# Performance work log

Hardware: AMD Instinct MI355X
Metric: run time of the kernel (lower is better)

The kernel has to match this reference:

```python
import jax, jax.numpy as jnp
import numpy as np

NEG_INF = -jnp.inf


def conv2d(x, w, b, stride, pad):
    # x: [B,C,H,W], w: [O,I,kh,kw]
    y = jax.lax.conv_general_dilated(
        x, w, window_strides=(stride, stride),
        padding=[(pad, pad), (pad, pad)],
        dimension_numbers=('NCHW', 'OIHW', 'NCHW'))
    return y + b[None, :, None, None]


def maxpool3s2(x):
    return jax.lax.reduce_window(x, -jnp.inf, jax.lax.max,
                                 (1, 1, 3, 3), (1, 1, 2, 2), 'VALID')


def setup_inputs() -> dict:
    key = jax.random.key(0)
    ks = jax.random.split(key, 20)
    s = 0.02
    B, C, H, W = 64, 3, 224, 224
    D, HID, OUT, E = 9216, 288, 1000, 8   # feature_dim, hidden_dim, output_dim, n_experts
    GH = 72                               # gate hidden = hidden_dim // 4
    inp = {
        'x':   jax.random.normal(ks[0], (B, C, H, W), jnp.float32),
        'c1w': s * jax.random.normal(ks[1], (64, 3, 11, 11), jnp.float32),
        'c1b': jnp.zeros((64,), jnp.float32),
        'c2w': s * jax.random.normal(ks[2], (192, 64, 5, 5), jnp.float32),
        'c2b': jnp.zeros((192,), jnp.float32),
        'c3w': s * jax.random.normal(ks[3], (384, 192, 3, 3), jnp.float32),
        'c3b': jnp.zeros((384,), jnp.float32),
        'c4w': s * jax.random.normal(ks[4], (256, 384, 3, 3), jnp.float32),
        'c4b': jnp.zeros((256,), jnp.float32),
        'c5w': s * jax.random.normal(ks[5], (256, 256, 3, 3), jnp.float32),
        'c5b': jnp.zeros((256,), jnp.float32),
        'gw1': s * jax.random.normal(ks[6], (D, GH), jnp.float32),
        'gb1': jnp.zeros((GH,), jnp.float32),
        'gw2': s * jax.random.normal(ks[7], (GH, E), jnp.float32),
        'gb2': jnp.zeros((E,), jnp.float32),
        'ew1': s * jax.random.normal(ks[8], (E, D, HID), jnp.float32),
        'eb1': jnp.zeros((E, HID), jnp.float32),
        'ew2': s * jax.random.normal(ks[9], (E, HID, HID // 2), jnp.float32),
        'eb2': jnp.zeros((E, HID // 2), jnp.float32),
        'ew3': s * jax.random.normal(ks[10], (E, HID // 2, OUT), jnp.float32),
        'eb3': jnp.zeros((E, OUT), jnp.float32),
    }
    return inp


def reference(x, c1w, c1b, c2w, c2b, c3w, c3b, c4w, c4b, c5w, c5b,
              gw1, gb1, gw2, gb2, ew1, eb1, ew2, eb2, ew3, eb3):
    # ---- AlexNet-style feature extractor (224 branch) ----
    h = jax.nn.relu(conv2d(x, c1w, c1b, 4, 2))   # [B,64,55,55]
    h = maxpool3s2(h)                             # [B,64,27,27]
    h = jax.nn.relu(conv2d(h, c2w, c2b, 1, 2))   # [B,192,27,27]
    h = maxpool3s2(h)                             # [B,192,13,13]
    h = jax.nn.relu(conv2d(h, c3w, c3b, 1, 1))   # [B,384,13,13]
    h = jax.nn.relu(conv2d(h, c4w, c4b, 1, 1))   # [B,256,13,13]
    h = jax.nn.relu(conv2d(h, c5w, c5b, 1, 1))   # [B,256,13,13]
    h = maxpool3s2(h)                             # [B,256,6,6]
    # AdaptiveAvgPool2d((6,6)) on a 6x6 input is the identity.
    feat = h.reshape(h.shape[0], -1)              # [B,9216]

    # ---- Gate: top-2 routing (eval mode: no noise, no dropout) ----
    g = jax.nn.relu(feat @ gw1 + gb1)             # [B,72]
    logits = g @ gw2 + gb2                        # [B,8]
    topv, topi = jax.lax.top_k(logits, 2)         # [B,2]
    topw = jax.nn.softmax(topv, axis=-1)          # softmax over top-2 only
    B = logits.shape[0]
    gates = jnp.zeros_like(logits).at[jnp.arange(B)[:, None], topi].set(topw)  # [B,8]

    # ---- Dense per-expert 3-layer MLP over full batch (as in source) ----
    h1 = jax.nn.relu(jnp.einsum('bd,edh->ebh', feat, ew1) + eb1[:, None, :])   # [E,B,288]
    h2 = jax.nn.relu(jnp.einsum('ebh,ehk->ebk', h1, ew2) + eb2[:, None, :])    # [E,B,144]
    eo = jnp.einsum('ebk,eko->ebo', h2, ew3) + eb3[:, None, :]                 # [E,B,1000]
    # Weighted combine; gates are zero for non-top-2 experts, matching the
    # masked accumulation loop in the torch forward.
    out = jnp.einsum('ebo,be->bo', eo, gates)     # [B,1000]
    return out
```

## Files before the change

kernel.cpp:

```cpp
#include <hip/hip_runtime.h>
#include <math.h>

#define TPB 256

typedef short s16x8 __attribute__((ext_vector_type(8)));
typedef short s16x4 __attribute__((ext_vector_type(4)));
typedef float f32x4 __attribute__((ext_vector_type(4)));

__device__ inline void bsplit(float x, short& h, short& l){
  union { float f; unsigned u; } a, hf, rf;
  a.f = x;
  unsigned hu = (a.u + 0x7FFFu + ((a.u >> 16) & 1u)) >> 16;
  h = (short)hu;
  hf.u = hu << 16;
  rf.f = x - hf.f;
  l = (short)((rf.u + 0x7FFFu + ((rf.u >> 16) & 1u)) >> 16);
}
__device__ inline float b2f(short s){
  union { unsigned u; float f; } x;
  x.u = ((unsigned)(unsigned short)s) << 16;
  return x.f;
}

__global__ __launch_bounds__(TPB) void wsplit_k(
    const float* __restrict__ w, short* __restrict__ wh, short* __restrict__ wl,
    int C, int O, int ntap, int total)
{
  int idx = blockIdx.x*TPB + threadIdx.x;
  if (idx >= total) return;
  int c   = idx % C;
  int t2  = idx / C;
  int oc  = t2 % O;
  int tap = t2 / O;
  float x = w[((size_t)oc*C + c)*ntap + tap];
  short h, l; bsplit(x, h, l);
  int tile = oc >> 4, ln = oc & 15;
  int S    = ntap*(C >> 5);
  int sl   = tap*(C >> 5) + (c >> 5);
  int lg   = (c >> 3) & 3, j = c & 7;
  size_t dst = (((size_t)tile*S + sl)*64 + lg*16 + ln)*8 + j;
  wh[dst] = h; wl[dst] = l;
}

__global__ __launch_bounds__(TPB) void wsplit1_k(
    const float* __restrict__ w, short* __restrict__ wh, short* __restrict__ wl)
{
  int idx = blockIdx.x*TPB + threadIdx.x;
  if (idx >= 64*576) return;
  int k  = idx % 576;
  int oc = idx / 576;
  int g  = k >> 4, kw = k & 15;
  int c  = g / 12, kh = g % 12;
  float x = 0.f;
  if (kh < 11 && kw < 11)
    x = w[((size_t)oc*3 + c)*121 + kh*11 + kw];
  short h, l; bsplit(x, h, l);
  int m = oc >> 4, ln = oc & 15;
  int s = k >> 5, r = k & 31;
  int lg = r >> 3, j = r & 7;
  size_t dst = (((size_t)m*18 + s)*64 + lg*16 + ln)*8 + j;
  wh[dst] = h; wl[dst] = l;
}

__global__ __launch_bounds__(TPB) void wtrans_k(
    const float* __restrict__ w, float* __restrict__ wT, int K, int O)
{
  int idx = blockIdx.x*TPB + threadIdx.x;
  if (idx >= K*O) return;
  int oc = idx % O;
  int k  = idx / O;
  wT[idx] = w[(size_t)oc*K + k];
}

#define C1W 240
__global__ __launch_bounds__(256, 2) void conv1p_k(
    const float* __restrict__ in, const short* __restrict__ whi,
    const short* __restrict__ wlo, const float* __restrict__ bias,
    short* __restrict__ yh, short* __restrict__ yl)
{
  __shared__ __align__(16) short lds[2][57*C1W + 84];
  const int tid = threadIdx.x;
  const int r  = blockIdx.x;
  const int b  = blockIdx.y;
  const int nt = tid >> 6;
  const int ln = tid & 15;
  const int lg = (tid & 63) >> 4;
  const int lane = tid & 63;
  const int ow = nt*16 + ln;

  const float* ip = in + (size_t)b*3*224*224;
  for (int i = tid; i < 57*59; i += 256){
    int plane = i / 59;
    int p     = i % 59;
    int c = plane / 19, ri = plane % 19;
    int ih = 8*r - 2 + ri;
    int col0 = p*4;
    const float* rowp = (ih >= 0 && ih < 224) ? ip + (size_t)c*50176 + (size_t)ih*224 : nullptr;
    short h[4], l[4];
    #pragma unroll
    for (int j=0;j<4;++j){
      int iw = col0 + j - 2;
      float v = (rowp && iw >= 0 && iw < 224) ? rowp[iw] : 0.f;
      bsplit(v, h[j], l[j]);
    }
    s16x4 hv = {h[0],h[1],h[2],h[3]}, lv = {l[0],l[1],l[2],l[3]};
    *reinterpret_cast<s16x4*>(&lds[0][plane*C1W + col0]) = hv;
    *reinterpret_cast<s16x4*>(&lds[1][plane*C1W + col0]) = lv;
  }
  __syncthreads();

  f32x4 acc[3][4];
  #pragma unroll
  for (int m=0;m<4;++m){
    const float4 bv = *reinterpret_cast<const float4*>(bias + m*16 + lg*4);
    #pragma unroll
    for (int sub=0;sub<3;++sub)
      acc[sub][m] = (f32x4){bv.x, bv.y, bv.z, bv.w};
  }

  s16x8 ah[4], al[4], ahn[4], aln[4];
  #pragma unroll
  for (int m=0;m<4;++m){
    size_t ao = (((size_t)m*18 + 0)*64 + lane)*8;
    ah[m] = *reinterpret_cast<const s16x8*>(whi + ao);
    al[m] = *reinterpret_cast<const s16x8*>(wlo + ao);
  }

  #pragma unroll 1
  for (int s=0; s<18; ++s){
    if (s < 17){
      #pragma unroll
      for (int m=0;m<4;++m){
        size_t ao = (((size_t)m*18 + s + 1)*64 + lane)*8;
        ahn[m] = *reinterpret_cast<const s16x8*>(whi + ao);
        aln[m] = *reinterpret_cast<const s16x8*>(wlo + ao);
      }
    }
    int g  = 2*s + (lg >> 1);
    int c  = g / 12, kh = g % 12;
    int khp = (kh < 11) ? kh : 10;
    #pragma unroll
    for (int sub=0;sub<3;++sub){
      int plane = c*19 + 4*sub + khp;
      int base  = plane*C1W + ow*4 + (lg & 1)*8;
      s16x4 h0 = *reinterpret_cast<const s16x4*>(&lds[0][base]);
      s16x4 h1 = *reinterpret_cast<const s16x4*>(&lds[0][base+4]);
      s16x4 l0 = *reinterpret_cast<const s16x4*>(&lds[1][base]);
      s16x4 l1 = *reinterpret_cast<const s16x4*>(&lds[1][base+4]);
      s16x8 bh = __builtin_shufflevector(h0, h1, 0,1,2,3,4,5,6,7);
      s16x8 bl = __builtin_shufflevector(l0, l1, 0,1,2,3,4,5,6,7);
      #pragma unroll
      for (int m=0;m<4;++m){
        acc[sub][m] = __builtin_amdgcn_mfma_f32_16x16x32_bf16(al[m], bh, acc[sub][m], 0,0,0);
        acc[sub][m] = __builtin_amdgcn_mfma_f32_16x16x32_bf16(ah[m], bl, acc[sub][m], 0,0,0);
        acc[sub][m] = __builtin_amdgcn_mfma_f32_16x16x32_bf16(ah[m], bh, acc[sub][m], 0,0,0);
      }
    }
    #pragma unroll
    for (int m=0;m<4;++m){ ah[m] = ahn[m]; al[m] = aln[m]; }
  }

  __syncthreads();
  float* convbuf = (float*)&lds[0][0];
  if (ow < 55){
    #pragma unroll
    for (int sub=0;sub<3;++sub)
      #pragma unroll
      for (int m=0;m<4;++m)
        #pragma unroll
        for (int rr=0;rr<4;++rr){
          int oc = m*16 + lg*4 + rr;
          convbuf[(sub*64 + oc)*57 + ow] = fmaxf(acc[sub][m][rr], 0.f);
        }
  }
  __syncthreads();

  for (int i = tid; i < 27*64; i += 256){
    int pw = i >> 6, c = i & 63;
    float m = -INFINITY;
    #pragma unroll
    for (int sub=0;sub<3;++sub)
      #pragma unroll
      for (int j=0;j<3;++j)
        m = fmaxf(m, convbuf[(sub*64 + c)*57 + 2*pw + j]);
    short h, l; bsplit(m, h, l);
    size_t o = ((size_t)b*729 + r*27 + pw)*64 + c;
    yh[o] = h; yl[o] = l;
  }
}

__global__ __launch_bounds__(256, 3) void conv2m_k(
    const short* __restrict__ xh, const short* __restrict__ xl,
    const short* __restrict__ whi, const short* __restrict__ wlo,
    const float* __restrict__ bias, short* __restrict__ yh, short* __restrict__ yl)
{
  __shared__ __align__(16) short lds[2][217*40];
  const int tid = threadIdx.x;
  const int rg  = blockIdx.x;
  const int b   = blockIdx.y;
  const int wid = tid >> 6;
  const int ln  = tid & 15;
  const int lg  = (tid & 63) >> 4;
  const int lane = tid & 63;
  const int oc0 = wid*48;
  const int r0  = rg*3;

  int sb[6], nn[6];
  #pragma unroll
  for (int t=0;t<6;++t){
    int n = t*16 + ln;
    nn[t] = n;
    int ohl = n / 27, ow = n % 27;
    sb[t] = (n < 81) ? (ohl*31 + ow) : 0;
  }

  f32x4 acc[3][6];
  #pragma unroll
  for (int m=0;m<3;++m){
    const float4 bv = *reinterpret_cast<const float4*>(bias + oc0 + m*16 + lg*4);
    #pragma unroll
    for (int t=0;t<6;++t) acc[m][t] = (f32x4){bv.x, bv.y, bv.z, bv.w};
  }

  #pragma unroll 1
  for (int c0=0; c0<64; c0+=32){
    __syncthreads();
    for (int i = tid; i < 217*4; i += 256){
      int sp = i >> 2, v = i & 3;
      int pr = sp/31, pc = sp%31;
      int ih = r0 - 2 + pr, iw = pc - 2;
      s16x8 hv = {0,0,0,0,0,0,0,0}, lv = {0,0,0,0,0,0,0,0};
      if (ih >= 0 && ih < 27 && iw >= 0 && iw < 27){
        size_t o = ((size_t)b*729 + ih*27 + iw)*64 + c0 + v*8;
        hv = *reinterpret_cast<const s16x8*>(xh + o);
        lv = *reinterpret_cast<const s16x8*>(xl + o);
      }
      *reinterpret_cast<s16x8*>(&lds[0][sp*40 + v*8]) = hv;
      *reinterpret_cast<s16x8*>(&lds[1][sp*40 + v*8]) = lv;
    }
    __syncthreads();

    const size_t tstr = 50*512;
    const size_t abase = ((size_t)(wid*3)*50 + (c0 >> 5))*512 + (size_t)lane*8;
    s16x8 ah0 = *reinterpret_cast<const s16x8*>(whi + abase);
    s16x8 ah1 = *reinterpret_cast<const s16x8*>(whi + abase + tstr);
    s16x8 ah2 = *reinterpret_cast<const s16x8*>(whi + abase + 2*tstr);
    s16x8 al0 = *reinterpret_cast<const s16x8*>(wlo + abase);
    s16x8 al1 = *reinterpret_cast<const s16x8*>(wlo + abase + tstr);
    s16x8 al2 = *reinterpret_cast<const s16x8*>(wlo + abase + 2*tstr);

    #pragma unroll 1
    for (int tap=0; tap<25; ++tap){
      s16x8 nh0=ah0, nh1=ah1, nh2=ah2, nl0=al0, nl1=al1, nl2=al2;
      if (tap < 24){
        size_t ao = abase + (size_t)(tap+1)*2*512;
        nh0 = *reinterpret_cast<const s16x8*>(whi + ao);
        nh1 = *reinterpret_cast<const s16x8*>(whi + ao + tstr);
        nh2 = *reinterpret_cast<const s16x8*>(whi + ao + 2*tstr);
        nl0 = *reinterpret_cast<const s16x8*>(wlo + ao);
        nl1 = *reinterpret_cast<const s16x8*>(wlo + ao + tstr);
        nl2 = *reinterpret_cast<const s16x8*>(wlo + ao + 2*tstr);
      }
      const int toff = (tap/5)*31 + (tap%5);
      #pragma unroll
      for (int t=0;t<6;++t){
        int off = (sb[t] + toff)*40 + lg*8;
        s16x8 bh = *reinterpret_cast<const s16x8*>(&lds[0][off]);
        s16x8 bl = *reinterpret_cast<const s16x8*>(&lds[1][off]);
        acc[0][t] = __builtin_amdgcn_mfma_f32_16x16x32_bf16(al0, bh, acc[0][t], 0,0,0);
        acc[0][t] = __builtin_amdgcn_mfma_f32_16x16x32_bf16(ah0, bl, acc[0][t], 0,0,0);
        acc[0][t] = __builtin_amdgcn_mfma_f32_16x16x32_bf16(ah0, bh, acc[0][t], 0,0,0);
        acc[1][t] = __builtin_amdgcn_mfma_f32_16x16x32_bf16(al1, bh, acc[1][t], 0,0,0);
        acc[1][t] = __builtin_amdgcn_mfma_f32_16x16x32_bf16(ah1, bl, acc[1][t], 0,0,0);
        acc[1][t] = __builtin_amdgcn_mfma_f32_16x16x32_bf16(ah1, bh, acc[1][t], 0,0,0);
        acc[2][t] = __builtin_amdgcn_mfma_f32_16x16x32_bf16(al2, bh, acc[2][t], 0,0,0);
        acc[2][t] = __builtin_amdgcn_mfma_f32_16x16x32_bf16(ah2, bl, acc[2][t], 0,0,0);
        acc[2][t] = __builtin_amdgcn_mfma_f32_16x16x32_bf16(ah2, bh, acc[2][t], 0,0,0);
      }
      ah0=nh0; ah1=nh1; ah2=nh2; al0=nl0; al1=nl1; al2=nl2;
    }
  }

  #pragma unroll
  for (int m=0;m<3;++m)
    #pragma unroll
    for (int t=0;t<6;++t){
      if (nn[t] < 81){
        int gsp = r0*27 + nn[t];
        size_t base = ((size_t)b*729 + gsp)*192 + oc0 + m*16 + lg*4;
        short h[4], l[4];
        #pragma unroll
        for (int r=0;r<4;++r) bsplit(fmaxf(acc[m][t][r], 0.f), h[r], l[r]);
        s16x4 hv = {h[0],h[1],h[2],h[3]}, lv = {l[0],l[1],l[2],l[3]};
        *reinterpret_cast<s16x4*>(yh + base) = hv;
        *reinterpret_cast<s16x4*>(yl + base) = lv;
      }
    }
}

__global__ __launch_bounds__(TPB) void pool2_k(
    const short* __restrict__ xh, const short* __restrict__ xl,
    short* __restrict__ yh, short* __restrict__ yl)
{
  int i = blockIdx.x*TPB + threadIdx.x;
  if (i >= 64*169*192) return;
  int c = i % 192;
  int t = i / 192;
  int sp = t % 169;
  int b = t / 169;
  int r = sp/13, cc = sp%13;
  const short* ph = xh + (size_t)b*729*192 + c;
  const short* pl = xl + (size_t)b*729*192 + c;
  float m = -INFINITY;
  #pragma unroll
  for (int di=0;di<3;++di)
    #pragma unroll
    for (int dj=0;dj<3;++dj){
      size_t s = (size_t)((2*r+di)*27 + 2*cc+dj)*192;
      m = fmaxf(m, b2f(ph[s]) + b2f(pl[s]));
    }
  short h, l; bsplit(m, h, l);
  yh[i] = h; yl[i] = l;
}

template<int C,int O>
__global__ __launch_bounds__(256, 3) void conv3m_k(
    const short* __restrict__ xh, const short* __restrict__ xl,
    const short* __restrict__ whi, const short* __restrict__ wlo,
    const float* __restrict__ bias, short* __restrict__ yh, short* __restrict__ yl)
{
  __shared__ __align__(16) short lds[2][225*40];
  const int tid = threadIdx.x;
  const int b   = blockIdx.y;
  const int wid = tid >> 6;
  const int ln  = tid & 15;
  const int lg  = (tid & 63) >> 4;
  const int lane = tid & 63;
  const int tileIdx = blockIdx.x*2 + (wid & 1);
  const int oc0 = tileIdx*16;
  const int ng  = wid >> 1;
  const int tbase  = ng ? 6 : 0;
  const int ntiles = ng ? 5 : 6;
  const int S3 = 9*(C/32);

  int sb[6], nn[6];
  #pragma unroll
  for (int t=0;t<6;++t){
    int n = (tbase + t)*16 + ln;
    nn[t] = n;
    int oh = n / 13, ow = n % 13;
    sb[t] = (n < 169) ? (oh*15 + ow) : 0;
  }

  f32x4 acc[6];
  const float4 bv = *reinterpret_cast<const float4*>(bias + oc0 + lg*4);
  #pragma unroll
  for (int t=0;t<6;++t) acc[t] = (f32x4){bv.x, bv.y, bv.z, bv.w};

  #pragma unroll 1
  for (int c0=0; c0<C; c0+=32){
    __syncthreads();
    for (int i = tid; i < 225*4; i += 256){
      int sp = i >> 2, v = i & 3;
      int r = sp/15, cc = sp%15;
      s16x8 hv = {0,0,0,0,0,0,0,0}, lv = {0,0,0,0,0,0,0,0};
      if (r >= 1 && r <= 13 && cc >= 1 && cc <= 13){
        size_t o = ((size_t)b*169 + (r-1)*13 + (cc-1))*C + c0 + v*8;
        hv = *reinterpret_cast<const s16x8*>(xh + o);
        lv = *reinterpret_cast<const s16x8*>(xl + o);
      }
      *reinterpret_cast<s16x8*>(&lds[0][sp*40 + v*8]) = hv;
      *reinterpret_cast<s16x8*>(&lds[1][sp*40 + v*8]) = lv;
    }
    __syncthreads();

    const size_t tb = (size_t)tileIdx*S3 + (c0 >> 5);
    s16x8 ah = *reinterpret_cast<const s16x8*>(whi + (tb*64 + lane)*8);
    s16x8 al = *reinterpret_cast<const s16x8*>(wlo + (tb*64 + lane)*8);
    #pragma unroll 1
    for (int tap=0; tap<9; ++tap){
      s16x8 ahn = ah, aln = al;
      if (tap < 8){
        size_t ao = ((tb + (size_t)(tap+1)*(C/32))*64 + lane)*8;
        ahn = *reinterpret_cast<const s16x8*>(whi + ao);
        aln = *reinterpret_cast<const s16x8*>(wlo + ao);
      }
      const int toff = (tap/3)*15 + (tap%3);
      #pragma unroll
      for (int t=0;t<6;++t){
        if (t < ntiles){
          int off = (sb[t] + toff)*40 + lg*8;
          s16x8 bh = *reinterpret_cast<const s16x8*>(&lds[0][off]);
          s16x8 bl = *reinterpret_cast<const s16x8*>(&lds[1][off]);
          acc[t] = __builtin_amdgcn_mfma_f32_16x16x32_bf16(al, bh, acc[t], 0,0,0);
          acc[t] = __builtin_amdgcn_mfma_f32_16x16x32_bf16(ah, bl, acc[t], 0,0,0);
          acc[t] = __builtin_amdgcn_mfma_f32_16x16x32_bf16(ah, bh, acc[t], 0,0,0);
        }
      }
      ah = ahn; al = aln;
    }
  }

  #pragma unroll
  for (int t=0;t<6;++t){
    if (t < ntiles && nn[t] < 169){
      size_t base = ((size_t)b*169 + nn[t])*O + oc0 + lg*4;
      short h[4], l[4];
      #pragma unroll
      for (int r=0;r<4;++r) bsplit(fmaxf(acc[t][r], 0.f), h[r], l[r]);
      s16x4 hv = {h[0],h[1],h[2],h[3]}, lv = {l[0],l[1],l[2],l[3]};
      *reinterpret_cast<s16x4*>(yh + base) = hv;
      *reinterpret_cast<s16x4*>(yl + base) = lv;
    }
  }
}

__global__ __launch_bounds__(TPB) void pool3_k(
    const short* __restrict__ xh, const short* __restrict__ xl,
    float* __restrict__ feat)
{
  int i = blockIdx.x*TPB + threadIdx.x;
  if (i >= 64*9216) return;
  int d = i % 9216;
  int b = i / 9216;
  int c = d / 36;
  int sp = d % 36;
  int r = sp/6, cc = sp%6;
  const short* ph = xh + (size_t)b*169*256 + c;
  const short* pl = xl + (size_t)b*169*256 + c;
  float m = -INFINITY;
  #pragma unroll
  for (int di=0;di<3;++di)
    #pragma unroll
    for (int dj=0;dj<3;++dj){
      size_t s = (size_t)((2*r+di)*13 + 2*cc+dj)*256;
      m = fmaxf(m, b2f(ph[s]) + b2f(pl[s]));
    }
  feat[i] = m;
}

__global__ __launch_bounds__(TPB) void featsplit_k(
    const float* __restrict__ feat, short* __restrict__ fbh, short* __restrict__ fbl)
{
  int idx = blockIdx.x*TPB + threadIdx.x;
  if (idx >= 589824) return;
  int j = idx & 7;
  int lane = (idx >> 3) & 63;
  int nt = (idx >> 9) & 3;
  int s = idx >> 11;
  int b = nt*16 + (lane & 15);
  int d = s*32 + (lane >> 4)*8 + j;
  short h, l; bsplit(feat[(size_t)b*9216 + d], h, l);
  fbh[idx] = h; fbl[idx] = l;
}

__global__ __launch_bounds__(256) void gate1_k(
    const float* __restrict__ feat, const float* __restrict__ gw1T,
    const float* __restrict__ gb1, float* __restrict__ g)
{
  const int b    = blockIdx.x;
  const int h    = blockIdx.y*4 + (threadIdx.x >> 6);
  const int lane = threadIdx.x & 63;
  const float* f = feat + (size_t)b*9216;
  const float* w = gw1T + (size_t)h*9216;
  float s = 0.f;
  #pragma unroll
  for (int it=0; it<36; ++it){
    int d = it*256 + lane*4;
    float4 fv = *reinterpret_cast<const float4*>(f + d);
    float4 wv = *reinterpret_cast<const float4*>(w + d);
    s = fmaf(fv.x, wv.x, s);
    s = fmaf(fv.y, wv.y, s);
    s = fmaf(fv.z, wv.z, s);
    s = fmaf(fv.w, wv.w, s);
  }
  #pragma unroll
  for (int off=32; off; off>>=1) s += __shfl_down(s, off, 64);
  if (lane == 0) g[(size_t)b*72 + h] = fmaxf(s + gb1[h], 0.f);
}

__global__ __launch_bounds__(128) void gate2_k(
    const float* __restrict__ g, const float* __restrict__ gw2,
    const float* __restrict__ gb2, float* __restrict__ gates)
{
  const int b = blockIdx.x;
  const int tid = threadIdx.x;
  __shared__ float gs[72];
  __shared__ float logits[8];
  if (tid < 72) gs[tid] = g[(size_t)b*72 + tid];
  __syncthreads();
  if (tid < 8) {
    float acc = gb2[tid];
    for (int j=0;j<72;++j)
      acc = fmaf(gs[j], gw2[(size_t)j*8 + tid], acc);
    logits[tid] = acc;
  }
  __syncthreads();
  if (tid == 0) {
    int i1 = 0; float v1 = logits[0];
    for (int e=1;e<8;++e) if (logits[e] > v1) { v1 = logits[e]; i1 = e; }
    int i2 = -1; float v2 = -INFINITY;
    for (int e=0;e<8;++e) { if (e==i1) continue; if (logits[e] > v2) { v2 = logits[e]; i2 = e; } }
    float z  = expf(v2 - v1);
    float w1 = 1.f / (1.f + z);
    float w2 = z   / (1.f + z);
    float* gr = gates + (size_t)b*8;
    for (int e=0;e<8;++e) gr[e] = 0.f;
    gr[i1] = w1;
    gr[i2] = w2;
  }
}

__global__ __launch_bounds__(256, 4) void eh1m_k(
    const float* __restrict__ ew1, const short* __restrict__ fbh,
    const short* __restrict__ fbl, float* __restrict__ part)
{
  __shared__ __align__(16) short wh_l[32*88];
  __shared__ __align__(16) short wl_l[32*88];
  const int m2 = blockIdx.x;
  const int e  = blockIdx.y;
  const int ks = blockIdx.z;
  const int tid = threadIdx.x;
  const int nt = tid >> 6;
  const int ln = tid & 15;
  const int lg = (tid & 63) >> 4;
  const int lane = tid & 63;

  f32x4 acc[2] = {(f32x4){0.f,0.f,0.f,0.f},(f32x4){0.f,0.f,0.f,0.f}};

  const float* wsrc = ew1 + (size_t)e*9216*288 + (size_t)m2*32;
  const int d0 = ks*576;

  #pragma unroll 1
  for (int st=0; st<9; ++st){
    __syncthreads();
    {
      int drow = tid >> 2;
      int h0 = (tid & 3)*8;
      const float* src = wsrc + (size_t)(d0 + st*64 + drow)*288 + h0;
      float4 v0 = *reinterpret_cast<const float4*>(src);
      float4 v1 = *reinterpret_cast<const float4*>(src+4);
      float vv[8] = {v0.x,v0.y,v0.z,v0.w,v1.x,v1.y,v1.z,v1.w};
      #pragma unroll
      for (int k=0;k<8;++k){
        short h, l; bsplit(vv[k], h, l);
        wh_l[(h0+k)*88 + drow] = h;
        wl_l[(h0+k)*88 + drow] = l;
      }
    }
    __syncthreads();
    int sg = (d0 + st*64) >> 5;
    #pragma unroll
    for (int sl=0; sl<2; ++sl){
      size_t bo = ((size_t)(sg+sl)*4 + nt)*512 + (size_t)lane*8;
      s16x8 bh = *reinterpret_cast<const s16x8*>(fbh + bo);
      s16x8 bl = *reinterpret_cast<const s16x8*>(fbl + bo);
      #pragma unroll
      for (int m=0;m<2;++m){
        int ao = (m*16 + ln)*88 + sl*32 + lg*8;
        s16x8 ah = *reinterpret_cast<const s16x8*>(&wh_l[ao]);
        s16x8 al = *reinterpret_cast<const s16x8*>(&wl_l[ao]);
        acc[m] = __builtin_amdgcn_mfma_f32_16x16x32_bf16(al, bh, acc[m], 0,0,0);
        acc[m] = __builtin_amdgcn_mfma_f32_16x16x32_bf16(ah, bl, acc[m], 0,0,0);
        acc[m] = __builtin_amdgcn_mfma_f32_16x16x32_bf16(ah, bh, acc[m], 0,0,0);
      }
    }
  }
  #pragma unroll
  for (int m=0;m<2;++m){
    int h = m2*32 + m*16 + lg*4;
    int b = nt*16 + ln;
    float* pp = part + ((size_t)(ks*8+e)*288 + h)*64 + b;
    #pragma unroll
    for (int r=0;r<4;++r)
      pp[(size_t)r*64] = acc[m][r];
  }
}

__global__ __launch_bounds__(TPB) void eh1_reduce_k(
    const float* __restrict__ part, const float* __restrict__ eb1,
    float* __restrict__ h1)
{
  int idx = blockIdx.x*TPB + threadIdx.x;
  if (idx >= 8*288*64) return;
  int b = idx & 63;
  int h = (idx >> 6) % 288;
  int e = idx / (64*288);
  float a = eb1[(size_t)e*288 + h];
  #pragma unroll
  for (int s=0;s<16;++s)
    a += part[((size_t)(s*8+e)*288 + h)*64 + b];
  h1[((size_t)e*64 + b)*288 + h] = fmaxf(a, 0.f);
}

__global__ __launch_bounds__(TPB) void expert_h2_k(
    const float* __restrict__ h1, const float* __restrict__ ew2,
    const float* __restrict__ eb2, const float* __restrict__ gates,
    float* __restrict__ h2)
{
  int idx = blockIdx.x*TPB + threadIdx.x;
  if (idx >= 8*64*144) return;
  int k = idx % 144;
  int t = idx / 144;
  int b = t % 64;
  int e = t / 64;
  if (gates[(size_t)b*8 + e] == 0.f) return;
  float acc = eb2[(size_t)e*144 + k];
  const float* h = h1 + ((size_t)e*64 + b)*288;
  const float* w = ew2 + (size_t)e*288*144 + k;
  for (int d=0; d<288; ++d)
    acc = fmaf(h[d], w[(size_t)d*144], acc);
  h2[idx] = fmaxf(acc, 0.f);
}

__global__ __launch_bounds__(TPB) void expert_out_k(
    const float* __restrict__ h2, const float* __restrict__ ew3,
    const float* __restrict__ eb3, const float* __restrict__ gates,
    float* __restrict__ out)
{
  int idx = blockIdx.x*TPB + threadIdx.x;
  if (idx >= 64*1000) return;
  int o = idx % 1000;
  int b = idx / 1000;
  float acc = 0.f;
  const float* gr = gates + (size_t)b*8;
  for (int e=0;e<8;++e){
    float ge = gr[e];
    if (ge == 0.f) continue;
    float a = eb3[(size_t)e*1000 + o];
    const float* h = h2 + ((size_t)e*64 + b)*144;
    const float* w = ew3 + (size_t)e*144*1000 + o;
    for (int k=0;k<144;++k)
      a = fmaf(h[k], w[(size_t)k*1000], a);
    acc = fmaf(ge, a, acc);
  }
  out[idx] = acc;
}

static inline int nblk(long long n){ return (int)((n + TPB - 1) / TPB); }

extern "C" void kernel_launch(void* const* d_in, const int* in_sizes, int n_in,
                              void* d_out, int out_size, void* d_ws, size_t ws_size,
                              hipStream_t stream)
{
  const float* x   = (const float*)d_in[0];
  const float* c1w = (const float*)d_in[1];  const float* c1b = (const float*)d_in[2];
  const float* c2w = (const float*)d_in[3];  const float* c2b = (const float*)d_in[4];
  const float* c3w = (const float*)d_in[5];  const float* c3b = (const float*)d_in[6];
  const float* c4w = (const float*)d_in[7];  const float* c4b = (const float*)d_in[8];
  const float* c5w = (const float*)d_in[9];  const float* c5b = (const float*)d_in[10];
  const float* gw1 = (const float*)d_in[11]; const float* gb1 = (const float*)d_in[12];
  const float* gw2 = (const float*)d_in[13]; const float* gb2 = (const float*)d_in[14];
  const float* ew1 = (const float*)d_in[15]; const float* eb1 = (const float*)d_in[16];
  const float* ew2 = (const float*)d_in[17]; const float* eb2 = (const float*)d_in[18];
  const float* ew3 = (const float*)d_in[19]; const float* eb3 = (const float*)d_in[20];
  float* out = (float*)d_out;

  float* W = (float*)d_ws;
  short* X3H = (short*)W;
  short* X3L = X3H + 8957952;
  short* X5H = (short*)W;
  short* X5L = X5H + 4153344;
  short* X7H = (short*)W;
  short* X7L = X7H + 2768896;
  float* feat  = W + 5000000;
  short* FBH   = (short*)(W + 5600000);
  short* FBL   = (short*)(W + 5900000);
  float* part  = W + 6300000;
  short* WH2 = (short*)(W +  9000000);
  short* WL2 = WH2 + 307200;
  short* WH3 = (short*)(W +  9320000);
  short* WL3 = WH3 + 663552;
  short* WH4 = (short*)(W + 10000000);
  short* WL4 = WH4 + 884736;
  short* WH5 = (short*)(W + 10900000);
  short* WL5 = WH5 + 589824;
  float* GT1 = W + 11500000;
  short* X2H = (short*)(W + 12390400);
  short* X2L = X2H + 2985984;
  short* X4H = (short*)(W + 12390400);
  short* X4L = X4H + 2076672;
  short* X6H = (short*)(W + 12390400);
  short* X6L = X6H + 2768896;
  float* gates = W + 14000000;
  float* h1    = gates + 512;
  float* h2    = h1 + 147456;
  float* gbuf  = h2 + 73728;
  short* WH1 = (short*)(W + 15400000);
  short* WL1 = WH1 + 36864;
  (void)ws_size; (void)in_sizes; (void)n_in; (void)out_size;

  wsplit1_k<<<nblk(64LL*576), TPB, 0, stream>>>(c1w, WH1, WL1);
  conv1p_k<<<dim3(27,64), 256, 0, stream>>>(x, WH1, WL1, c1b, X2H, X2L);
  wsplit_k<<<nblk(25LL*192*64),  TPB, 0, stream>>>(c2w, WH2, WL2,  64, 192, 25, 25*192*64);
  wsplit_k<<<nblk(9LL*384*192),  TPB, 0, stream>>>(c3w, WH3, WL3, 192, 384,  9, 9*384*192);
  wsplit_k<<<nblk(9LL*256*384),  TPB, 0, stream>>>(c4w, WH4, WL4, 384, 256,  9, 9*256*384);
  wsplit_k<<<nblk(9LL*256*256),  TPB, 0, stream>>>(c5w, WH5, WL5, 256, 256,  9, 9*256*256);
  wtrans_k<<<nblk(72LL*9216),    TPB, 0, stream>>>(gw1, GT1, 72, 9216);

  conv2m_k<<<dim3(9,64), 256, 0, stream>>>(X2H, X2L, WH2, WL2, c2b, X3H, X3L);
  pool2_k<<<nblk(64LL*169*192), TPB, 0, stream>>>(X3H, X3L, X4H, X4L);
  conv3m_k<192,384><<<dim3(12,64), 256, 0, stream>>>(X4H, X4L, WH3, WL3, c3b, X5H, X5L);
  conv3m_k<384,256><<<dim3(8,64),  256, 0, stream>>>(X5H, X5L, WH4, WL4, c4b, X6H, X6L);
  conv3m_k<256,256><<<dim3(8,64),  256, 0, stream>>>(X6H, X6L, WH5, WL5, c5b, X7H, X7L);
  pool3_k<<<nblk(64LL*9216), TPB, 0, stream>>>(X7H, X7L, feat);

  gate1_k<<<dim3(64,18), 256, 0, stream>>>(feat, GT1, gb1, gbuf);
  gate2_k<<<64, 128, 0, stream>>>(gbuf, gw2, gb2, gates);

  featsplit_k<<<nblk(589824LL), TPB, 0, stream>>>(feat, FBH, FBL);
  eh1m_k<<<dim3(9,8,16), 256, 0, stream>>>(ew1, FBH, FBL, part);
  eh1_reduce_k<<<nblk(8LL*288*64), TPB, 0, stream>>>(part, eb1, h1);
  expert_h2_k<<<nblk(8LL*64*144), TPB, 0, stream>>>(h1, ew2, eb2, gates, h2);
  expert_out_k<<<nblk(64LL*1000), TPB, 0, stream>>>(h2, ew3, eb3, gates, out);
}
```

Measured before the change: 513.0 us.

## Split conv1 blocks across width halves and output-channel halves per wave

```diff
diff --git a/kernel.cpp b/kernel.cpp
--- a/kernel.cpp
+++ b/kernel.cpp
@@ -72,26 +72,30 @@
   wT[idx] = w[(size_t)oc*K + k];
 }
 
-#define C1W 240
-__global__ __launch_bounds__(256, 2) void conv1p_k(
+#define CW1 128
+__global__ __launch_bounds__(256, 4) void conv1p_k(
     const float* __restrict__ in, const short* __restrict__ whi,
     const short* __restrict__ wlo, const float* __restrict__ bias,
     short* __restrict__ yh, short* __restrict__ yl)
 {
-  __shared__ __align__(16) short lds[2][57*C1W + 84];
+  __shared__ __align__(16) short lds[2][57*CW1 + 176];
   const int tid = threadIdx.x;
   const int r  = blockIdx.x;
   const int b  = blockIdx.y;
-  const int nt = tid >> 6;
+  const int hf = blockIdx.z;
+  const int wid = tid >> 6;
+  const int ntl = wid & 1;
+  const int och = wid >> 1;
   const int ln = tid & 15;
   const int lg = (tid & 63) >> 4;
   const int lane = tid & 63;
-  const int ow = nt*16 + ln;
+  const int lw = ntl*16 + ln;
+  const int iwbase = hf*112 - 2;
 
   const float* ip = in + (size_t)b*3*224*224;
-  for (int i = tid; i < 57*59; i += 256){
-    int plane = i / 59;
-    int p     = i % 59;
+  for (int i = tid; i < 57*32; i += 256){
+    int plane = i >> 5;
+    int p     = i & 31;
     int c = plane / 19, ri = plane % 19;
     int ih = 8*r - 2 + ri;
     int col0 = p*4;
@@ -99,29 +103,29 @@
     short h[4], l[4];
     #pragma unroll
     for (int j=0;j<4;++j){
-      int iw = col0 + j - 2;
+      int iw = iwbase + col0 + j;
       float v = (rowp && iw >= 0 && iw < 224) ? rowp[iw] : 0.f;
       bsplit(v, h[j], l[j]);
     }
     s16x4 hv = {h[0],h[1],h[2],h[3]}, lv = {l[0],l[1],l[2],l[3]};
-    *reinterpret_cast<s16x4*>(&lds[0][plane*C1W + col0]) = hv;
-    *reinterpret_cast<s16x4*>(&lds[1][plane*C1W + col0]) = lv;
+    *reinterpret_cast<s16x4*>(&lds[0][plane*CW1 + col0]) = hv;
+    *reinterpret_cast<s16x4*>(&lds[1][plane*CW1 + col0]) = lv;
   }
   __syncthreads();
 
-  f32x4 acc[3][4];
-  #pragma unroll
-  for (int m=0;m<4;++m){
-    const float4 bv = *reinterpret_cast<const float4*>(bias + m*16 + lg*4);
+  f32x4 acc[3][2];
+  #pragma unroll
+  for (int m=0;m<2;++m){
+    const float4 bv = *reinterpret_cast<const float4*>(bias + och*32 + m*16 + lg*4);
     #pragma unroll
     for (int sub=0;sub<3;++sub)
       acc[sub][m] = (f32x4){bv.x, bv.y, bv.z, bv.w};
   }
 
-  s16x8 ah[4], al[4], ahn[4], aln[4];
-  #pragma unroll
-  for (int m=0;m<4;++m){
-    size_t ao = (((size_t)m*18 + 0)*64 + lane)*8;
+  s16x8 ah[2], al[2], ahn[2], aln[2];
+  #pragma unroll
+  for (int m=0;m<2;++m){
+    size_t ao = (((size_t)(och*2+m)*18 + 0)*64 + lane)*8;
     ah[m] = *reinterpret_cast<const s16x8*>(whi + ao);
     al[m] = *reinterpret_cast<const s16x8*>(wlo + ao);
   }
@@ -130,8 +134,8 @@
   for (int s=0; s<18; ++s){
     if (s < 17){
       #pragma unroll
-      for (int m=0;m<4;++m){
-        size_t ao = (((size_t)m*18 + s + 1)*64 + lane)*8;
+      for (int m=0;m<2;++m){
+        size_t ao = (((size_t)(och*2+m)*18 + s + 1)*64 + lane)*8;
         ahn[m] = *reinterpret_cast<const s16x8*>(whi + ao);
         aln[m] = *reinterpret_cast<const s16x8*>(wlo + ao);
       }
@@ -142,7 +146,7 @@
     #pragma unroll
     for (int sub=0;sub<3;++sub){
       int plane = c*19 + 4*sub + khp;
-      int base  = plane*C1W + ow*4 + (lg & 1)*8;
+      int base  = plane*CW1 + lw*4 + (lg & 1)*8;
       s16x4 h0 = *reinterpret_cast<const s16x4*>(&lds[0][base]);
       s16x4 h1 = *reinterpret_cast<const s16x4*>(&lds[0][base+4]);
       s16x4 l0 = *reinterpret_cast<const s16x4*>(&lds[1][base]);
@@ -150,40 +154,40 @@
       s16x8 bh = __builtin_shufflevector(h0, h1, 0,1,2,3,4,5,6,7);
       s16x8 bl = __builtin_shufflevector(l0, l1, 0,1,2,3,4,5,6,7);
       #pragma unroll
-      for (int m=0;m<4;++m){
+      for (int m=0;m<2;++m){
         acc[sub][m] = __builtin_amdgcn_mfma_f32_16x16x32_bf16(al[m], bh, acc[sub][m], 0,0,0);
         acc[sub][m] = __builtin_amdgcn_mfma_f32_16x16x32_bf16(ah[m], bl, acc[sub][m], 0,0,0);
         acc[sub][m] = __builtin_amdgcn_mfma_f32_16x16x32_bf16(ah[m], bh, acc[sub][m], 0,0,0);
       }
     }
     #pragma unroll
-    for (int m=0;m<4;++m){ ah[m] = ahn[m]; al[m] = aln[m]; }
+    for (int m=0;m<2;++m){ ah[m] = ahn[m]; al[m] = aln[m]; }
   }
 
   __syncthreads();
   float* convbuf = (float*)&lds[0][0];
-  if (ow < 55){
+  #pragma unroll
+  for (int sub=0;sub<3;++sub)
+    #pragma unroll
+    for (int m=0;m<2;++m)
+      #pragma unroll
+      for (int rr=0;rr<4;++rr){
+        int oc = och*32 + m*16 + lg*4 + rr;
+        convbuf[(sub*36 + lw)*65 + oc] = fmaxf(acc[sub][m][rr], 0.f);
+      }
+  __syncthreads();
+
+  const int npw = hf ? 13 : 14;
+  for (int i = tid; i < npw*64; i += 256){
+    int pwl = i >> 6, c = i & 63;
+    float m = -INFINITY;
     #pragma unroll
     for (int sub=0;sub<3;++sub)
       #pragma unroll
-      for (int m=0;m<4;++m)
-        #pragma unroll
-        for (int rr=0;rr<4;++rr){
-          int oc = m*16 + lg*4 + rr;
-          convbuf[(sub*64 + oc)*57 + ow] = fmaxf(acc[sub][m][rr], 0.f);
-        }
-  }
-  __syncthreads();
-
-  for (int i = tid; i < 27*64; i += 256){
-    int pw = i >> 6, c = i & 63;
-    float m = -INFINITY;
-    #pragma unroll
-    for (int sub=0;sub<3;++sub)
-      #pragma unroll
       for (int j=0;j<3;++j)
-        m = fmaxf(m, convbuf[(sub*64 + c)*57 + 2*pw + j]);
+        m = fmaxf(m, convbuf[(sub*36 + 2*pwl + j)*65 + c]);
     short h, l; bsplit(m, h, l);
+    int pw = hf*14 + pwl;
     size_t o = ((size_t)b*729 + r*27 + pw)*64 + c;
     yh[o] = h; yl[o] = l;
   }
@@ -691,7 +695,7 @@
   (void)ws_size; (void)in_sizes; (void)n_in; (void)out_size;
 
   wsplit1_k<<<nblk(64LL*576), TPB, 0, stream>>>(c1w, WH1, WL1);
-  conv1p_k<<<dim3(27,64), 256, 0, stream>>>(x, WH1, WL1, c1b, X2H, X2L);
+  conv1p_k<<<dim3(27,64,2), 256, 0, stream>>>(x, WH1, WL1, c1b, X2H, X2L);
   wsplit_k<<<nblk(25LL*192*64),  TPB, 0, stream>>>(c2w, WH2, WL2,  64, 192, 25, 25*192*64);
   wsplit_k<<<nblk(9LL*384*192),  TPB, 0, stream>>>(c3w, WH3, WL3, 192, 384,  9, 9*384*192);
   wsplit_k<<<nblk(9LL*256*384),  TPB, 0, stream>>>(c4w, WH4, WL4, 384, 256,  9, 9*256*384);
```

After: 500.5 us (median of 2 runs). -2.4%, faster.
